# Optimization experiments

Hardware: AMD Instinct MI355X
Metric: run time of the kernel (lower is better)

## Reference

```python
import jax, jax.numpy as jnp
import numpy as np

BETA = 0.99      # rootfind_module beta
TOL = 1e-3       # torch loop: while V(fx*a) - t > 0.001
MAX_ITER = 50    # safety cap (torch loop is uncapped but converges)


def _fhat(x, W1, b1, W2, b2):
    # x: (B,1,D) -> (B,1,D)
    h = jnp.tanh(x @ W1 + b1)
    return h @ W2 + b2


def _V_sample(z, Wv1, Wv2):
    # z: (1,D) -> scalar Lyapunov value
    h = jnp.tanh(z @ Wv1)
    y = h @ Wv2
    return jnp.sum(y * y) + 0.01 * jnp.sum(z * z)


def _V(z, Wv1, Wv2):
    # z: (B,1,D) -> (B,1,1)
    h = jnp.tanh(z @ Wv1)
    y = h @ Wv2
    v = jnp.sum(y * y, axis=(-2, -1)) + 0.01 * jnp.sum(z * z, axis=(-2, -1))
    return v[:, None, None]


def _newton_step(fhatx, target, alpha, Wv1, Wv2):
    # newton_iter.forward: F = alpha - (V(fhatx*alpha) - target) / dV/dalpha
    z = fhatx * alpha                                  # (B,1,D)
    Vz = _V(z, Wv1, Wv2)                               # (B,1,1)
    gradV = jax.vmap(jax.grad(_V_sample), in_axes=(0, None, None))(z, Wv1, Wv2)
    dV_da = jnp.sum(gradV * fhatx, axis=(-2, -1))[:, None, None]
    return alpha - (Vz - target) / dV_da


def _rootfind(fhatx, target, Wv1, Wv2):
    # batched, masked replacement of torch per-sample Python while loops
    B = fhatx.shape[0]
    alpha0 = jnp.ones((B, 1, 1), fhatx.dtype)

    def cond(carry):
        i, alpha = carry
        resid = _V(fhatx * alpha, Wv1, Wv2) - target
        return jnp.logical_and(i < MAX_ITER, jnp.any(resid > TOL))

    def body(carry):
        i, alpha = carry
        resid = _V(fhatx * alpha, Wv1, Wv2) - target
        new_alpha = _newton_step(fhatx, target, alpha, Wv1, Wv2)
        alpha = jnp.where(resid > TOL, new_alpha, alpha)  # only unconverged samples move
        return (i + 1, alpha)

    _, alpha = jax.lax.while_loop(cond, body, (jnp.int32(0), alpha0))
    return alpha


def setup_inputs() -> dict:
    key = jax.random.key(0)
    ks = jax.random.split(key, 5)
    B, D, H, HV, VO = 8192, 512, 2048, 512, 256
    s = 0.02
    return {
        "x": jax.random.normal(ks[0], (B, 1, D), jnp.float32),
        "W1": jax.random.normal(ks[1], (D, H), jnp.float32) * s,
        "b1": jnp.zeros((H,), jnp.float32),
        "W2": jax.random.normal(ks[2], (H, D), jnp.float32) * s,
        "b2": jnp.zeros((D,), jnp.float32),
        "Wv1": jax.random.normal(ks[3], (D, HV), jnp.float32) * s,
        "Wv2": jax.random.normal(ks[4], (HV, VO), jnp.float32) * s,
    }


def reference(x, W1, b1, W2, b2, Wv1, Wv2):
    fhatx = _fhat(x, W1, b1, W2, b2)        # (B,1,D)
    target = BETA * _V(x, Wv1, Wv2)         # (B,1,1)
    alpha = _rootfind(fhatx, target, Wv1, Wv2)
    return fhatx * alpha                    # x_root, (B,1,D)
```

## Files before the change

kernel.cpp:

```cpp
#include <hip/hip_runtime.h>
#include <hip/hip_bf16.h>
#include <stdint.h>
#include <stddef.h>

typedef __bf16 bf16_t;
typedef __bf16 bf16x8 __attribute__((ext_vector_type(8)));
typedef __bf16 bf16x4 __attribute__((ext_vector_type(4)));
typedef float  f32x4  __attribute__((ext_vector_type(4)));

#define NB 8192
#define ND 512
#define NH 2048
#define NHV 512
#define NVO 256
#define RF_TOL 1e-3f
#define NEWTON_MAX 16

typedef const __attribute__((address_space(1))) void gvoid_t;
typedef __attribute__((address_space(3))) void lvoid_t;

__device__ __forceinline__ void gload_lds16(const void* g, void* l) {
  __builtin_amdgcn_global_load_lds((gvoid_t*)g, (lvoid_t*)l, 16, 0, 0);
}

__device__ __forceinline__ float fast_tanhf(float x) {
  x = fminf(fmaxf(x, -15.0f), 15.0f);
  float e = __expf(2.0f * x);
  return (e - 1.0f) * __builtin_amdgcn_rcpf(e + 1.0f);
}

struct GJob {
  const bf16_t* A;
  const bf16_t* Bt;
  const float*  bias;
  bf16_t* Cbf;
  float*  Cf;
  int N, K, nbx, tanh_act;
};

template<int BM, bool SWZ>
__global__ __launch_bounds__(256, 4)
void gemm_kernel(GJob j0, GJob j1)
{
  constexpr int MI = BM / 32;
  __shared__ bf16_t As[BM * 64];
  __shared__ bf16_t Bs[128 * 64];

  int bx0, by;
  if (SWZ) {
    int f = (int)blockIdx.y * (int)gridDim.x + (int)blockIdx.x;
    const int nwg = (int)gridDim.x * (int)gridDim.y;
    f = (f & 7) * (nwg >> 3) + (f >> 3);
    bx0 = f % (int)gridDim.x;
    by  = f / (int)gridDim.x;
  } else {
    bx0 = (int)blockIdx.x;
    by  = (int)blockIdx.y;
  }

  const bool first = bx0 < j0.nbx;
  const GJob jb = first ? j0 : j1;
  const int bx = bx0 - (first ? 0 : j0.nbx);
  const int K = jb.K, N = jb.N;

  const int t = threadIdx.x, lane = t & 63, w = t >> 6;
  const int wm = w >> 1, wn = w & 1;
  const int la = lane & 15, lg = lane >> 4;
  const size_t m0 = (size_t)by * BM, n0 = (size_t)bx * 128;

  size_t soffA[MI], soffB[4]; int doff[4];
#pragma unroll
  for (int j = 0; j < 4; ++j) {
    const int off = t * 16 + j * 4096;
    const int r = off >> 7, c = off & 127;
    const size_t so = (size_t)r * K + ((c ^ ((r & 7) << 4)) >> 1);
    if (j < MI) soffA[j] = so;
    soffB[j] = so;
    doff[j] = off;
  }
  const bf16_t* Ab = jb.A + m0 * K;
  const bf16_t* Bb = jb.Bt + n0 * K;

  int abyte[MI][2], bbyte[4][2];
#pragma unroll
  for (int ks = 0; ks < 2; ++ks) {
#pragma unroll
    for (int i = 0; i < MI; ++i) {
      const int ra = wm * (BM / 2) + i * 16 + la;
      abyte[i][ks] = ra * 128 + ((ks * 64 + lg * 16) ^ ((ra & 7) << 4));
    }
#pragma unroll
    for (int j = 0; j < 4; ++j) {
      const int rb = wn * 64 + j * 16 + la;
      bbyte[j][ks] = rb * 128 + ((ks * 64 + lg * 16) ^ ((rb & 7) << 4));
    }
  }

  f32x4 acc[MI][4] = {};
  const int nsteps = K >> 6;

  for (int ts = 0; ts < nsteps; ++ts) {
    const int k0 = ts << 6;
#pragma unroll
    for (int j = 0; j < MI; ++j)
      gload_lds16(Ab + soffA[j] + k0, (char*)As + doff[j]);
#pragma unroll
    for (int j = 0; j < 4; ++j)
      gload_lds16(Bb + soffB[j] + k0, (char*)Bs + doff[j]);
    __syncthreads();

    bf16x8 afr[MI][2], bfr[4][2];
#pragma unroll
    for (int ks = 0; ks < 2; ++ks) {
#pragma unroll
      for (int i = 0; i < MI; ++i)
        afr[i][ks] = *(const bf16x8*)((const char*)As + abyte[i][ks]);
#pragma unroll
      for (int j = 0; j < 4; ++j)
        bfr[j][ks] = *(const bf16x8*)((const char*)Bs + bbyte[j][ks]);
    }
#pragma unroll
    for (int ks = 0; ks < 2; ++ks)
#pragma unroll
      for (int i = 0; i < MI; ++i)
#pragma unroll
        for (int j = 0; j < 4; ++j)
          acc[i][j] = __builtin_amdgcn_mfma_f32_16x16x32_bf16(afr[i][ks], bfr[j][ks], acc[i][j], 0, 0, 0);
    __syncthreads();
  }

#pragma unroll
  for (int i = 0; i < MI; ++i) {
#pragma unroll
    for (int j = 0; j < 4; ++j) {
      const size_t col = n0 + wn * 64 + j * 16 + la;
      const float bv = jb.bias ? jb.bias[col] : 0.0f;
#pragma unroll
      for (int r = 0; r < 4; ++r) {
        const size_t row = m0 + wm * (BM / 2) + i * 16 + lg * 4 + r;
        float v = acc[i][j][r] + bv;
        if (jb.tanh_act) v = fast_tanhf(v);
        if (jb.Cbf) jb.Cbf[row * N + col] = (bf16_t)v;
        if (jb.Cf)  jb.Cf [row * N + col] = v;
      }
    }
  }
}

__device__ __forceinline__ void tr_body(const float* __restrict__ src, bf16_t* __restrict__ dst,
                                        int R, int C, int bidx, float (*tile)[33]) {
  const int tilesx = C >> 5;
  const int bi = (bidx / tilesx) << 5, bj = (bidx % tilesx) << 5;
  const int t = threadIdx.x, tx = t & 31, ty = t >> 5;
#pragma unroll
  for (int r = ty; r < 32; r += 8)
    tile[r][tx] = src[(size_t)(bi + r) * C + (bj + tx)];
  __syncthreads();
#pragma unroll
  for (int r = ty; r < 32; r += 8)
    dst[(size_t)(bj + r) * R + (bi + tx)] = (bf16_t)tile[tx][r];
}

__global__ void prep_kernel(const float* __restrict__ x, bf16_t* __restrict__ xbf, float* __restrict__ xsq,
                            const float* __restrict__ W1, bf16_t* __restrict__ w1t,
                            const float* __restrict__ W2, bf16_t* __restrict__ w2t,
                            const float* __restrict__ Wv1, bf16_t* __restrict__ wv1t,
                            const float* __restrict__ Wv2, bf16_t* __restrict__ wv2t)
{
  __shared__ float tile[32][33];
  const int b = blockIdx.x;
  if (b < 1024)      tr_body(W1, w1t, 512, 2048, b, tile);
  else if (b < 2048) tr_body(W2, w2t, 2048, 512, b - 1024, tile);
  else if (b < 2304) tr_body(Wv1, wv1t, 512, 512, b - 2048, tile);
  else if (b < 2432) tr_body(Wv2, wv2t, 512, 256, b - 2304, tile);
  else {
    const int t = threadIdx.x;
    const int row = (b - 2432) * 4 + (t >> 6), l = t & 63;
    const float4* sr = (const float4*)(x + (size_t)row * ND);
    bf16x4* dw = (bf16x4*)(xbf + (size_t)row * ND);
    float s = 0.0f;
#pragma unroll
    for (int c = l; c < ND / 4; c += 64) {
      float4 v = sr[c];
      s = fmaf(v.x, v.x, fmaf(v.y, v.y, fmaf(v.z, v.z, fmaf(v.w, v.w, s))));
      bf16x4 o;
      o[0] = (bf16_t)v.x; o[1] = (bf16_t)v.y; o[2] = (bf16_t)v.z; o[3] = (bf16_t)v.w;
      dw[c] = o;
    }
#pragma unroll
    for (int m = 32; m; m >>= 1) s += __shfl_xor(s, m);
    if (l == 0) xsq[row] = s;
  }
}

__global__ __launch_bounds__(512, 1)
void newton_kernel(const bf16_t* __restrict__ fbf, const bf16_t* __restrict__ wv1t,
                   const bf16_t* __restrict__ Wv2t,
                   const float* __restrict__ yx, const float* __restrict__ xsq,
                   const float* __restrict__ fhat, float* __restrict__ out)
{
  __shared__ alignas(16) bf16_t hs[32 * 512];
  __shared__ alignas(16) bf16_t es[32 * 512];
  __shared__ float red[8][32][2];
  __shared__ float alpha_s[32], fsq_s[32], tgt_s[32];
  __shared__ int notdone_s;

  const int t = threadIdx.x, lane = t & 63, w = t >> 6;
  const int la = lane & 15, lg = lane >> 4;
  const int s_base = blockIdx.x * 32;
  const int arow = lane & 31, ahi = lane >> 5;

  {
    const int row = t >> 4, c0 = (t & 15) * 4;
    float s = 0.0f;
#pragma unroll
    for (int i = 0; i < 4; ++i) {
      const int k8 = c0 + i;
      bf16x8 v = *(const bf16x8*)(fbf + (size_t)(s_base + row) * ND + k8 * 8);
#pragma unroll
      for (int q = 0; q < 8; ++q) { float f = (float)v[q]; s = fmaf(f, f, s); }
      *(bf16x8*)((char*)hs + (row << 10) + ((k8 ^ (row & 7)) << 4)) = v;
    }
    s += __shfl_xor(s, 1); s += __shfl_xor(s, 2); s += __shfl_xor(s, 4); s += __shfl_xor(s, 8);
    if ((t & 15) == 0) fsq_s[row] = s;
  }
  {
    const int smp = t >> 4;
    const float4* yp = (const float4*)(yx + (size_t)(s_base + smp) * NVO + (t & 15) * 16);
    float s = 0.0f;
#pragma unroll
    for (int i = 0; i < 4; ++i) {
      float4 v = yp[i];
      s = fmaf(v.x, v.x, fmaf(v.y, v.y, fmaf(v.z, v.z, fmaf(v.w, v.w, s))));
    }
    s += __shfl_xor(s, 1); s += __shfl_xor(s, 2); s += __shfl_xor(s, 4); s += __shfl_xor(s, 8);
    if ((t & 15) == 0) tgt_s[smp] = 0.99f * (s + 0.01f * xsq[s_base + smp]);
  }
  if (t < 32) alpha_s[t] = 1.0f;
  __syncthreads();

  f32x4 uacc[2][4] = {};
#pragma unroll
  for (int k = 0; k < 16; ++k) {
    bf16x8 afr[2];
#pragma unroll
    for (int mt = 0; mt < 2; ++mt) {
      const int row = mt * 16 + la;
      afr[mt] = *(const bf16x8*)((const char*)hs + (row << 10) + (((k * 4 + lg) ^ (row & 7)) << 4));
    }
#pragma unroll
    for (int nt = 0; nt < 4; ++nt) {
      const bf16x8 b = *(const bf16x8*)(wv1t + (size_t)(w * 64 + nt * 16 + la) * ND + k * 32 + lg * 8);
#pragma unroll
      for (int mt = 0; mt < 2; ++mt)
        uacc[mt][nt] = __builtin_amdgcn_mfma_f32_16x16x32_bf16(afr[mt], b, uacc[mt][nt], 0, 0, 0);
    }
  }

#pragma unroll
  for (int mt = 0; mt < 2; ++mt)
#pragma unroll
    for (int nt = 0; nt < 4; ++nt)
#pragma unroll
      for (int r = 0; r < 4; ++r) {
        const int row = mt * 16 + lg * 4 + r;
        const int col = w * 64 + nt * 16 + la;
        *(bf16_t*)((char*)es + (row << 10) + (((col >> 3) ^ (row & 7)) << 4) + (col & 7) * 2)
            = (bf16_t)uacc[mt][nt][r];
      }
  __syncthreads();

  bf16x8 ureg[4];
#pragma unroll
  for (int i = 0; i < 4; ++i) {
    const int k8 = w * 8 + ahi * 4 + i;
    ureg[i] = *(const bf16x8*)((const char*)es + (arow << 10) + ((k8 ^ (arow & 7)) << 4));
  }

  bf16x8 bfr[2][16];
#pragma unroll
  for (int nt = 0; nt < 2; ++nt) {
    const bf16_t* bp = Wv2t + (size_t)(w * 32 + nt * 16 + la) * NHV + lg * 8;
#pragma unroll
    for (int k = 0; k < 16; ++k)
      bfr[nt][k] = *(const bf16x8*)(bp + k * 32);
  }
  __syncthreads();

  for (int it = 0; it < NEWTON_MAX; ++it) {
    {
      const float c2 = 2.0f * alpha_s[arow];
#pragma unroll
      for (int i = 0; i < 4; ++i) {
        const int k8 = w * 8 + ahi * 4 + i;
        const int byte = (arow << 10) + ((k8 ^ (arow & 7)) << 4);
        bf16x8 uv = ureg[i], hf, ef;
#pragma unroll
        for (int q = 0; q < 8; ++q) {
          float u = (float)uv[q];
          float e = __expf(c2 * u);
          float h = (e - 1.0f) * __builtin_amdgcn_rcpf(e + 1.0f);
          hf[q] = (bf16_t)h;
          ef[q] = (bf16_t)(u * (1.0f - h * h));
        }
        *(bf16x8*)((char*)hs + byte) = hf;
        *(bf16x8*)((char*)es + byte) = ef;
      }
    }
    __syncthreads();

    f32x4 accy[2][2] = {};
    f32x4 accw[2][2] = {};
#pragma unroll
    for (int k = 0; k < 16; ++k) {
#pragma unroll
      for (int mt = 0; mt < 2; ++mt) {
        const int row = mt * 16 + la;
        const int byte = (row << 10) + (((k * 4 + lg) ^ (row & 7)) << 4);
        bf16x8 hf = *(const bf16x8*)((const char*)hs + byte);
        bf16x8 ef = *(const bf16x8*)((const char*)es + byte);
#pragma unroll
        for (int nt = 0; nt < 2; ++nt) {
          accy[mt][nt] = __builtin_amdgcn_mfma_f32_16x16x32_bf16(hf, bfr[nt][k], accy[mt][nt], 0, 0, 0);
          accw[mt][nt] = __builtin_amdgcn_mfma_f32_16x16x32_bf16(ef, bfr[nt][k], accw[mt][nt], 0, 0, 0);
        }
      }
    }

#pragma unroll
    for (int mt = 0; mt < 2; ++mt) {
#pragma unroll
      for (int r = 0; r < 4; ++r) {
        float sy = 0.0f, sw = 0.0f;
#pragma unroll
        for (int nt = 0; nt < 2; ++nt) {
          float yv = accy[mt][nt][r], wv = accw[mt][nt][r];
          sy = fmaf(yv, yv, sy);
          sw = fmaf(yv, wv, sw);
        }
        sy += __shfl_xor(sy, 1); sw += __shfl_xor(sw, 1);
        sy += __shfl_xor(sy, 2); sw += __shfl_xor(sw, 2);
        sy += __shfl_xor(sy, 4); sw += __shfl_xor(sw, 4);
        sy += __shfl_xor(sy, 8); sw += __shfl_xor(sw, 8);
        if (la == 0) {
          red[w][mt * 16 + lg * 4 + r][0] = sy;
          red[w][mt * 16 + lg * 4 + r][1] = sw;
        }
      }
    }
    __syncthreads();
    if (t < 32) {
      float SY = 0.0f, SW = 0.0f;
#pragma unroll
      for (int w8 = 0; w8 < 8; ++w8) {
        SY += red[w8][t][0];
        SW += red[w8][t][1];
      }
      float a = alpha_s[t];
      const float fs = fsq_s[t];
      const float V = SY + 0.01f * a * a * fs;
      const float dV = 2.0f * SW + 0.02f * a * fs;
      const float resid = V - tgt_s[t];
      const bool go = resid > RF_TOL;
      if (go) alpha_s[t] = a - resid / dV;
      const int nd = __any(go);
      if (t == 0) notdone_s = nd;
    }
    __syncthreads();
    if (!notdone_s) break;
  }

  {
    const int r = t >> 4;
    const int c4 = t & 15;
    const float a = alpha_s[r];
    const size_t rb = (size_t)(s_base + r) * ND;
    const float4* sp = (const float4*)(fhat + rb);
    float4* dp = (float4*)(out + rb);
#pragma unroll
    for (int jj = 0; jj < 8; ++jj) {
      float4 v = sp[c4 + jj * 16];
      v.x *= a; v.y *= a; v.z *= a; v.w *= a;
      dp[c4 + jj * 16] = v;
    }
  }
}

extern "C" void kernel_launch(void* const* d_in, const int* in_sizes, int n_in,
                              void* d_out, int out_size, void* d_ws, size_t ws_size,
                              hipStream_t stream)
{
  (void)in_sizes; (void)n_in; (void)out_size; (void)ws_size;
  const float* x   = (const float*)d_in[0];
  const float* W1  = (const float*)d_in[1];
  const float* b1  = (const float*)d_in[2];
  const float* W2  = (const float*)d_in[3];
  const float* b2  = (const float*)d_in[4];
  const float* Wv1 = (const float*)d_in[5];
  const float* Wv2 = (const float*)d_in[6];
  float* out = (float*)d_out;

  char* ws = (char*)d_ws;
  size_t off = 0;
  auto alloc = [&](size_t n) { char* p = ws + off; off += (n + 255) & ~(size_t)255; return p; };

  bf16_t* xbf  = (bf16_t*)alloc((size_t)NB * ND * 2);
  bf16_t* w1t  = (bf16_t*)alloc((size_t)NH * ND * 2);
  bf16_t* w2t  = (bf16_t*)alloc((size_t)ND * NH * 2);
  bf16_t* wv1t = (bf16_t*)alloc((size_t)NHV * ND * 2);
  bf16_t* wv2t = (bf16_t*)alloc((size_t)NVO * NHV * 2);
  bf16_t* h1   = (bf16_t*)alloc((size_t)NB * NH * 2);
  float*  fhat = (float*)alloc((size_t)NB * ND * 4);
  bf16_t* fbf  = (bf16_t*)alloc((size_t)NB * ND * 2);
  bf16_t* hx   = (bf16_t*)alloc((size_t)NB * NHV * 2);
  float*  yx   = (float*)alloc((size_t)NB * NVO * 4);
  float*  xsq  = (float*)alloc((size_t)NB * 4);

  prep_kernel<<<4480, 256, 0, stream>>>(x, xbf, xsq, W1, w1t, W2, w2t, Wv1, wv1t, Wv2, wv2t);

  GJob jh1 { xbf, w1t,  b1,      h1,  nullptr, NH,  ND, NH  / 128, 1 };
  GJob jhx { xbf, wv1t, nullptr, hx,  nullptr, NHV, ND, NHV / 128, 1 };
  gemm_kernel<128, true><<<dim3(NH / 128 + NHV / 128, NB / 128), 256, 0, stream>>>(jh1, jhx);

  GJob jf  { h1,  w2t,  b2,      fbf, fhat,    ND,  NH, ND  / 128, 0 };
  GJob jy  { hx,  wv2t, nullptr, nullptr, yx,  NVO, NHV, NVO / 128, 0 };
  gemm_kernel<64, true><<<dim3(ND / 128 + NVO / 128, NB / 64), 256, 0, stream>>>(jf, jy);

  newton_kernel<<<NB / 32, 512, 0, stream>>>(fbf, wv1t, wv2t, yx, xsq, fhat, out);
}
```

Measured before the change: 120.3 us.

## Fuse y·y row reduction into GEMM epilogue and move weight transposes into GEMM grid

The second GEMM's Wv2 branch now reduces its output to per-row sums of squares with atomics instead of storing the full fp32 yx matrix, and the Newton kernel reads only the scalar. The W2 and Wv2 transposes move from the prep kernel into extra blocks of the first GEMM launch, shrinking prep. This removes a large fp32 write and read and shortens the prep kernel, at the cost of atomic adds and a zero-init of the row-sum buffer.

```diff
diff --git a/kernel.cpp b/kernel.cpp
--- a/kernel.cpp
+++ b/kernel.cpp
@@ -35,12 +35,28 @@
   const float*  bias;
   bf16_t* Cbf;
   float*  Cf;
+  float*  rowsq;
   int N, K, nbx, tanh_act;
 };
 
-template<int BM, bool SWZ>
+__device__ __forceinline__ void tr_body(const float* __restrict__ src, bf16_t* __restrict__ dst,
+                                        int R, int C, int bidx, float (*tile)[33]) {
+  const int tilesx = C >> 5;
+  const int bi = (bidx / tilesx) << 5, bj = (bidx % tilesx) << 5;
+  const int t = threadIdx.x, tx = t & 31, ty = t >> 5;
+#pragma unroll
+  for (int r = ty; r < 32; r += 8)
+    tile[r][tx] = src[(size_t)(bi + r) * C + (bj + tx)];
+  __syncthreads();
+#pragma unroll
+  for (int r = ty; r < 32; r += 8)
+    dst[(size_t)(bj + r) * R + (bi + tx)] = (bf16_t)tile[tx][r];
+}
+
+template<int BM, bool SWZ, int TBX>
 __global__ __launch_bounds__(256, 4)
-void gemm_kernel(GJob j0, GJob j1)
+void gemm_kernel(GJob j0, GJob j1,
+                 const float* tw2, bf16_t* tw2t, const float* twv2, bf16_t* twv2t)
 {
   constexpr int MI = BM / 32;
   __shared__ bf16_t As[BM * 64];
@@ -58,6 +74,14 @@
     by  = (int)blockIdx.y;
   }
 
+  if (TBX > 0 && bx0 >= TBX) {
+    float (*tile)[33] = reinterpret_cast<float(*)[33]>(As);
+    const int idx = (bx0 - TBX) * (int)gridDim.y + by;
+    if (idx < 1024) tr_body(tw2, tw2t, 2048, 512, idx, tile);
+    else            tr_body(twv2, twv2t, 512, 256, idx - 1024, tile);
+    return;
+  }
+
   const bool first = bx0 < j0.nbx;
   const GJob jb = first ? j0 : j1;
   const int bx = bx0 - (first ? 0 : j0.nbx);
@@ -129,6 +153,22 @@
     __syncthreads();
   }
 
+  if (jb.rowsq) {
+#pragma unroll
+    for (int i = 0; i < MI; ++i) {
+#pragma unroll
+      for (int r = 0; r < 4; ++r) {
+        float s = 0.0f;
+#pragma unroll
+        for (int j = 0; j < 4; ++j) { float v = acc[i][j][r]; s = fmaf(v, v, s); }
+        s += __shfl_xor(s, 1); s += __shfl_xor(s, 2);
+        s += __shfl_xor(s, 4); s += __shfl_xor(s, 8);
+        if (la == 0)
+          atomicAdd(&jb.rowsq[m0 + wm * (BM / 2) + i * 16 + lg * 4 + r], s);
+      }
+    }
+    return;
+  }
 #pragma unroll
   for (int i = 0; i < MI; ++i) {
 #pragma unroll
@@ -147,35 +187,18 @@
   }
 }
 
-__device__ __forceinline__ void tr_body(const float* __restrict__ src, bf16_t* __restrict__ dst,
-                                        int R, int C, int bidx, float (*tile)[33]) {
-  const int tilesx = C >> 5;
-  const int bi = (bidx / tilesx) << 5, bj = (bidx % tilesx) << 5;
-  const int t = threadIdx.x, tx = t & 31, ty = t >> 5;
-#pragma unroll
-  for (int r = ty; r < 32; r += 8)
-    tile[r][tx] = src[(size_t)(bi + r) * C + (bj + tx)];
-  __syncthreads();
-#pragma unroll
-  for (int r = ty; r < 32; r += 8)
-    dst[(size_t)(bj + r) * R + (bi + tx)] = (bf16_t)tile[tx][r];
-}
-
 __global__ void prep_kernel(const float* __restrict__ x, bf16_t* __restrict__ xbf, float* __restrict__ xsq,
                             const float* __restrict__ W1, bf16_t* __restrict__ w1t,
-                            const float* __restrict__ W2, bf16_t* __restrict__ w2t,
                             const float* __restrict__ Wv1, bf16_t* __restrict__ wv1t,
-                            const float* __restrict__ Wv2, bf16_t* __restrict__ wv2t)
+                            float* __restrict__ yxsq)
 {
   __shared__ float tile[32][33];
   const int b = blockIdx.x;
   if (b < 1024)      tr_body(W1, w1t, 512, 2048, b, tile);
-  else if (b < 2048) tr_body(W2, w2t, 2048, 512, b - 1024, tile);
-  else if (b < 2304) tr_body(Wv1, wv1t, 512, 512, b - 2048, tile);
-  else if (b < 2432) tr_body(Wv2, wv2t, 512, 256, b - 2304, tile);
+  else if (b < 1280) tr_body(Wv1, wv1t, 512, 512, b - 1024, tile);
   else {
     const int t = threadIdx.x;
-    const int row = (b - 2432) * 4 + (t >> 6), l = t & 63;
+    const int row = (b - 1280) * 4 + (t >> 6), l = t & 63;
     const float4* sr = (const float4*)(x + (size_t)row * ND);
     bf16x4* dw = (bf16x4*)(xbf + (size_t)row * ND);
     float s = 0.0f;
@@ -190,13 +213,14 @@
 #pragma unroll
     for (int m = 32; m; m >>= 1) s += __shfl_xor(s, m);
     if (l == 0) xsq[row] = s;
+    if (l == 1) yxsq[row] = 0.0f;
   }
 }
 
 __global__ __launch_bounds__(512, 1)
 void newton_kernel(const bf16_t* __restrict__ fbf, const bf16_t* __restrict__ wv1t,
                    const bf16_t* __restrict__ Wv2t,
-                   const float* __restrict__ yx, const float* __restrict__ xsq,
+                   const float* __restrict__ yxsq, const float* __restrict__ xsq,
                    const float* __restrict__ fhat, float* __restrict__ out)
 {
   __shared__ alignas(16) bf16_t hs[32 * 512];
@@ -224,19 +248,10 @@
     s += __shfl_xor(s, 1); s += __shfl_xor(s, 2); s += __shfl_xor(s, 4); s += __shfl_xor(s, 8);
     if ((t & 15) == 0) fsq_s[row] = s;
   }
-  {
-    const int smp = t >> 4;
-    const float4* yp = (const float4*)(yx + (size_t)(s_base + smp) * NVO + (t & 15) * 16);
-    float s = 0.0f;
-#pragma unroll
-    for (int i = 0; i < 4; ++i) {
-      float4 v = yp[i];
-      s = fmaf(v.x, v.x, fmaf(v.y, v.y, fmaf(v.z, v.z, fmaf(v.w, v.w, s))));
-    }
-    s += __shfl_xor(s, 1); s += __shfl_xor(s, 2); s += __shfl_xor(s, 4); s += __shfl_xor(s, 8);
-    if ((t & 15) == 0) tgt_s[smp] = 0.99f * (s + 0.01f * xsq[s_base + smp]);
-  }
-  if (t < 32) alpha_s[t] = 1.0f;
+  if (t < 32) {
+    alpha_s[t] = 1.0f;
+    tgt_s[t] = 0.99f * (yxsq[s_base + t] + 0.01f * xsq[s_base + t]);
+  }
   __syncthreads();
 
   f32x4 uacc[2][4] = {};
@@ -413,18 +428,18 @@
   float*  fhat = (float*)alloc((size_t)NB * ND * 4);
   bf16_t* fbf  = (bf16_t*)alloc((size_t)NB * ND * 2);
   bf16_t* hx   = (bf16_t*)alloc((size_t)NB * NHV * 2);
-  float*  yx   = (float*)alloc((size_t)NB * NVO * 4);
   float*  xsq  = (float*)alloc((size_t)NB * 4);
-
-  prep_kernel<<<4480, 256, 0, stream>>>(x, xbf, xsq, W1, w1t, W2, w2t, Wv1, wv1t, Wv2, wv2t);
-
-  GJob jh1 { xbf, w1t,  b1,      h1,  nullptr, NH,  ND, NH  / 128, 1 };
-  GJob jhx { xbf, wv1t, nullptr, hx,  nullptr, NHV, ND, NHV / 128, 1 };
-  gemm_kernel<128, true><<<dim3(NH / 128 + NHV / 128, NB / 128), 256, 0, stream>>>(jh1, jhx);
-
-  GJob jf  { h1,  w2t,  b2,      fbf, fhat,    ND,  NH, ND  / 128, 0 };
-  GJob jy  { hx,  wv2t, nullptr, nullptr, yx,  NVO, NHV, NVO / 128, 0 };
-  gemm_kernel<64, true><<<dim3(ND / 128 + NVO / 128, NB / 64), 256, 0, stream>>>(jf, jy);
-
-  newton_kernel<<<NB / 32, 512, 0, stream>>>(fbf, wv1t, wv2t, yx, xsq, fhat, out);
-}
+  float*  yxsq = (float*)alloc((size_t)NB * 4);
+
+  prep_kernel<<<3328, 256, 0, stream>>>(x, xbf, xsq, W1, w1t, Wv1, wv1t, yxsq);
+
+  GJob jh1 { xbf, w1t,  b1,      h1,  nullptr, nullptr, NH,  ND, NH  / 128, 1 };
+  GJob jhx { xbf, wv1t, nullptr, hx,  nullptr, nullptr, NHV, ND, NHV / 128, 1 };
+  gemm_kernel<128, true, 20><<<dim3(38, NB / 128), 256, 0, stream>>>(jh1, jhx, W2, w2t, Wv2, wv2t);
+
+  GJob jf  { h1,  w2t,  b2,      fbf, fhat,    nullptr, ND,  NH, ND  / 128, 0 };
+  GJob jy  { hx,  wv2t, nullptr, nullptr, nullptr, yxsq, NVO, NHV, NVO / 128, 0 };
+  gemm_kernel<64, true, 0><<<dim3(ND / 128 + NVO / 128, NB / 64), 256, 0, stream>>>(jf, jy, nullptr, nullptr, nullptr, nullptr);
+
+  newton_kernel<<<NB / 32, 512, 0, stream>>>(fbf, wv1t, wv2t, yxsq, xsq, fhat, out);
+}
```

Result: faster. 115.3 us (-4.2%).
